# Optimization experiments

Measured on AMD Instinct MI355X. Metric: run time of the kernel, lower is better.

Reference implementation:

```python
import jax, jax.numpy as jnp
import numpy as np

DIM = 1024
N_HEADS = 16
HEAD_DIM = DIM // N_HEADS
SPARSITY = 0.8
SCALE = HEAD_DIM ** -0.5


def setup_inputs() -> dict:
    key = jax.random.key(0)
    ks = jax.random.split(key, 9)
    B, S = 2, 2048
    std = DIM ** -0.5
    return {
        "x": jax.random.normal(ks[0], (B, S, DIM), dtype=jnp.float32),
        "wq": jax.random.normal(ks[1], (DIM, DIM), dtype=jnp.float32) * std,
        "bq": jnp.zeros((DIM,), dtype=jnp.float32),
        "wk": jax.random.normal(ks[2], (DIM, DIM), dtype=jnp.float32) * std,
        "bk": jnp.zeros((DIM,), dtype=jnp.float32),
        "wv": jax.random.normal(ks[3], (DIM, DIM), dtype=jnp.float32) * std,
        "bv": jnp.zeros((DIM,), dtype=jnp.float32),
        "wo": jax.random.normal(ks[4], (DIM, DIM), dtype=jnp.float32) * std,
        "bo": jnp.zeros((DIM,), dtype=jnp.float32),
    }


def _attn(x, wq, bq, wk, bk, wv, bv, wo, bo):
    B, S, _ = x.shape
    # torch Linear: y = x @ W.T + b
    def proj(w, b):
        y = jnp.einsum('bsd,ed->bse', x, w) + b
        return y.reshape(B, S, N_HEADS, HEAD_DIM).transpose(0, 2, 1, 3)  # [B,H,S,hd]
    q, k, v = proj(wq, bq), proj(wk, bk), proj(wv, bv)
    scores = jnp.einsum('bhqd,bhkd->bhqk', q, k) * SCALE  # [B,H,S,S]
    # top-k sparsity: keep k = max(1, int(S*(1-sparsity))) largest per row
    kk = max(1, int(S * (1.0 - SPARSITY)))
    topk_vals, topk_idx = jax.lax.top_k(scores, kk)
    sparse = jnp.full_like(scores, -jnp.inf)
    sparse = jnp.put_along_axis(sparse, topk_idx, topk_vals, axis=-1, inplace=False)
    attn = jax.nn.softmax(sparse, axis=-1)  # dropout disabled (eval)
    out = jnp.einsum('bhqk,bhkd->bhqd', attn, v)
    out = out.transpose(0, 2, 1, 3).reshape(B, S, DIM)
    out = jnp.einsum('bsd,ed->bse', out, wo) + bo
    return out, attn


def reference(x, wq, bq, wk, bk, wv, bv, wo, bo):
    return _attn(x, wq, bq, wk, bk, wv, bv, wo, bo)
```

## Files before the change

### kernel.cpp

```cpp
#include <hip/hip_runtime.h>
#include <hip/hip_bf16.h>

#define DIMN 1024
#define NH 16
#define HD 64
#define SEQ 2048
#define BATCH 2
#define BHN (BATCH*NH)
#define MROWS (BATCH*SEQ)
#define KKEEP 409
#define SCALEF 0.125f
#define QROWS 16

typedef __attribute__((ext_vector_type(8))) short short8;
typedef __attribute__((ext_vector_type(4))) short short4v;
typedef __attribute__((ext_vector_type(4))) float f32x4;

#define MFMA(a,b,c) __builtin_amdgcn_mfma_f32_16x16x32_bf16(a,b,c,0,0,0)


static __device__ __forceinline__ short f2bf(float f) {
    __hip_bfloat16 h = __float2bfloat16(f);
    return *reinterpret_cast<short*>(&h);
}
static __device__ __forceinline__ float bf2f(short s) {
    __hip_bfloat16 h = *reinterpret_cast<__hip_bfloat16*>(&s);
    return __bfloat162float(h);
}
static __device__ __forceinline__ short8 ld8(const short* p) {
    return *reinterpret_cast<const short8*>(p);
}
static __device__ __forceinline__ float keyf(unsigned u) {
    unsigned fu = (u & 0x80000000u) ? (u ^ 0x80000000u) : ~u;
    return __uint_as_float(fu);
}
static __device__ __forceinline__ size_t tidx(int row, int k) {
    return (size_t)(row >> 4) * 16384 + (size_t)(k >> 5) * 512
         + ((((k >> 3) & 3) * 16 + (row & 15)) * 8) + (k & 7);
}

__global__ void conv_hilo_t(const float* __restrict__ in,
                            short* __restrict__ hi, short* __restrict__ lo, int rows) {
    const int total = rows * 256;
    for (int idx = blockIdx.x * blockDim.x + threadIdx.x; idx < total;
         idx += gridDim.x * blockDim.x) {
        const int row = idx >> 8;
        const int k = (idx & 255) * 4;
        float4 v = *reinterpret_cast<const float4*>(in + (size_t)row * DIMN + k);
        short4v h, l;
        #pragma unroll
        for (int j = 0; j < 4; ++j) {
            float f = (&v.x)[j];
            short hb = f2bf(f);
            h[j] = hb;
            l[j] = f2bf(f - bf2f(hb));
        }
        const size_t o = tidx(row, k);
        *reinterpret_cast<short4v*>(hi + o) = h;
        *reinterpret_cast<short4v*>(lo + o) = l;
    }
}

__global__ void conv_bf16_t(const float* __restrict__ in,
                            short* __restrict__ out, int rows) {
    const int total = rows * 256;
    for (int idx = blockIdx.x * blockDim.x + threadIdx.x; idx < total;
         idx += gridDim.x * blockDim.x) {
        const int row = idx >> 8;
        const int k = (idx & 255) * 4;
        float4 v = *reinterpret_cast<const float4*>(in + (size_t)row * DIMN + k);
        short4v o;
        o[0] = f2bf(v.x); o[1] = f2bf(v.y); o[2] = f2bf(v.z); o[3] = f2bf(v.w);
        *reinterpret_cast<short4v*>(out + tidx(row, k)) = o;
    }
}

__global__ __launch_bounds__(256) void qk_mfma(
    const short* __restrict__ xh, const short* __restrict__ xl,
    const short* __restrict__ wqh, const short* __restrict__ wql, const float* __restrict__ bq,
    const short* __restrict__ wkh, const short* __restrict__ wkl, const float* __restrict__ bk,
    short* __restrict__ qhi, short* __restrict__ qlo,
    short* __restrict__ khi, short* __restrict__ klo)
{
    const int z = blockIdx.z;
    const short* wh = z ? wkh : wqh;
    const short* wl = z ? wkl : wql;
    const float* bias = z ? bk : bq;
    short* dhi = z ? khi : qhi;
    short* dlo = z ? klo : qlo;

    const int tid  = threadIdx.x;
    const int wv_  = tid >> 6, lane = tid & 63;
    const int r    = lane & 15, kg = lane >> 4;
    const int m_base = blockIdx.x * 128 + wv_ * 32;
    const int n_base = blockIdx.y * 64;
    const int mtile0 = blockIdx.x * 8 + wv_ * 2;
    const int ntile0 = blockIdx.y * 4;

    f32x4 acc[2][4] = {};

    for (int ks = 0; ks < 32; ++ks) {
        short8 ah0 = ld8(xh + (size_t)mtile0 * 16384 + ks * 512 + lane * 8);
        short8 al0 = ld8(xl + (size_t)mtile0 * 16384 + ks * 512 + lane * 8);
        short8 ah1 = ld8(xh + (size_t)(mtile0 + 1) * 16384 + ks * 512 + lane * 8);
        short8 al1 = ld8(xl + (size_t)(mtile0 + 1) * 16384 + ks * 512 + lane * 8);
        #pragma unroll
        for (int nf = 0; nf < 4; ++nf) {
            short8 bh = ld8(wh + (size_t)(ntile0 + nf) * 16384 + ks * 512 + lane * 8);
            short8 bl = ld8(wl + (size_t)(ntile0 + nf) * 16384 + ks * 512 + lane * 8);
            acc[0][nf] = MFMA(ah0, bh, acc[0][nf]);
            acc[0][nf] = MFMA(ah0, bl, acc[0][nf]);
            acc[0][nf] = MFMA(al0, bh, acc[0][nf]);
            acc[1][nf] = MFMA(ah1, bh, acc[1][nf]);
            acc[1][nf] = MFMA(ah1, bl, acc[1][nf]);
            acc[1][nf] = MFMA(al1, bh, acc[1][nf]);
        }
    }

    const int h = blockIdx.y;
    #pragma unroll
    for (int mf = 0; mf < 2; ++mf)
        #pragma unroll
        for (int nf = 0; nf < 4; ++nf)
            #pragma unroll
            for (int i = 0; i < 4; ++i) {
                const int m  = m_base + mf * 16 + kg * 4 + i;
                const int nn = n_base + nf * 16 + r;
                const float val = acc[mf][nf][i] + bias[nn];
                const int b_ = m >> 11, s = m & 2047;
                const int hd = nf * 16 + r;
                const size_t idx = (size_t)(b_ * NH + h) * 131072
                    + (size_t)(s >> 4) * 1024 + (hd >> 5) * 512
                    + ((((hd >> 3) & 3) * 16 + (s & 15)) * 8) + (hd & 7);
                const short hb = f2bf(val);
                dhi[idx] = hb;
                dlo[idx] = f2bf(val - bf2f(hb));
            }
}

__global__ __launch_bounds__(256) void v_mfma(
    const short* __restrict__ xh, const short* __restrict__ xl,
    const short* __restrict__ wvb, const float* __restrict__ bv,
    short* __restrict__ vt)
{
    const int tid  = threadIdx.x;
    const int wv_  = tid >> 6, lane = tid & 63;
    const int r    = lane & 15, kg = lane >> 4;
    const int m_base = blockIdx.x * 128 + wv_ * 32;
    const int n_base = blockIdx.y * 64;
    const int mtile0 = blockIdx.x * 8 + wv_ * 2;
    const int ntile0 = blockIdx.y * 4;

    f32x4 acc[2][4] = {};

    for (int ks = 0; ks < 32; ++ks) {
        short8 ah0 = ld8(xh + (size_t)mtile0 * 16384 + ks * 512 + lane * 8);
        short8 al0 = ld8(xl + (size_t)mtile0 * 16384 + ks * 512 + lane * 8);
        short8 ah1 = ld8(xh + (size_t)(mtile0 + 1) * 16384 + ks * 512 + lane * 8);
        short8 al1 = ld8(xl + (size_t)(mtile0 + 1) * 16384 + ks * 512 + lane * 8);
        #pragma unroll
        for (int nf = 0; nf < 4; ++nf) {
            short8 b = ld8(wvb + (size_t)(ntile0 + nf) * 16384 + ks * 512 + lane * 8);
            acc[0][nf] = MFMA(ah0, b, acc[0][nf]);
            acc[0][nf] = MFMA(al0, b, acc[0][nf]);
            acc[1][nf] = MFMA(ah1, b, acc[1][nf]);
            acc[1][nf] = MFMA(al1, b, acc[1][nf]);
        }
    }

    const int h = blockIdx.y;
    #pragma unroll
    for (int mf = 0; mf < 2; ++mf)
        #pragma unroll
        for (int nf = 0; nf < 4; ++nf)
            #pragma unroll
            for (int i = 0; i < 4; ++i) {
                const int m  = m_base + mf * 16 + kg * 4 + i;
                const int nn = n_base + nf * 16 + r;
                const float val = acc[mf][nf][i] + bv[nn];
                const int b_ = m >> 11, s = m & 2047;
                const int hd = nf * 16 + r;
                const size_t idx = (size_t)(b_ * NH + h) * 131072
                    + (size_t)(hd >> 4) * 32768 + (size_t)(s >> 5) * 512
                    + ((((s >> 3) & 3) * 16 + (hd & 15)) * 8) + (s & 7);
                vt[idx] = f2bf(val);
            }
}

__global__ __launch_bounds__(512, 4) void fused_attn(
    const short* __restrict__ qh, const short* __restrict__ ql,
    const short* __restrict__ kh, const short* __restrict__ kl,
    const short* __restrict__ vtb, float* __restrict__ attn,
    short* __restrict__ ctxt)
{
    __shared__ __align__(16) char smem[32768];
    float* CT = (float*)(smem + 16384);

    const int tid = threadIdx.x;
    const int w   = tid >> 6, lane = tid & 63;
    const int r   = lane & 15, kg = lane >> 4;

    const int bid  = blockIdx.x;
    const int xcd  = bid & 7;
    const int slot = bid >> 3;
    const int bh   = xcd + 8 * (slot >> 7);
    const int qt   = slot & 127;
    const int q0   = qt * QROWS;

    const size_t qtbase = (size_t)bh * 131072 + (size_t)qt * 1024 + lane * 8;
    short8 a0h = ld8(qh + qtbase),       a0l = ld8(ql + qtbase);
    short8 a1h = ld8(qh + qtbase + 512), a1l = ld8(ql + qtbase + 512);

    unsigned u[2][32];

    auto STAGE = [&](int c, float* buf) {
        #pragma unroll
        for (int tt = 0; tt < 2; ++tt) {
            const int stile = c * 16 + w + 8 * tt;
            const size_t tb = (size_t)bh * 131072 + (size_t)stile * 1024 + lane * 8;
            short8 b0h = ld8(kh + tb);
            short8 b0l = ld8(kl + tb);
            short8 b1h = ld8(kh + tb + 512);
            short8 b1l = ld8(kl + tb + 512);
            f32x4 accA = {0.f, 0.f, 0.f, 0.f};
            f32x4 accB = {0.f, 0.f, 0.f, 0.f};
            accA = MFMA(a0h, b0h, accA);
            accB = MFMA(a1h, b1h, accB);
            accA = MFMA(a0h, b0l, accA);
            accB = MFMA(a1h, b1l, accB);
            accA = MFMA(a0l, b0h, accA);
            accB = MFMA(a1l, b1h, accB);
            const int j0c = (w + 8 * tt) * 16;
            #pragma unroll
            for (int i = 0; i < 4; ++i)
                buf[(kg * 4 + i) * 256 + j0c + r] = (accA[i] + accB[i]) * SCALEF;
        }
    };

    STAGE(0, (float*)smem);
    __syncthreads();
    #pragma unroll
    for (int c = 0; c < 8; ++c) {
        float* cur = (float*)(smem + ((c & 1) ? 16384 : 0));
        float* nxt = (float*)(smem + ((c & 1) ? 0 : 16384));
        if (c + 1 < 8) STAGE(c + 1, nxt);
        #pragma unroll
        for (int rr = 0; rr < 2; ++rr) {
            const float* src = cur + (w + 8 * rr) * 256;
            f32x4 v4 = *reinterpret_cast<const f32x4*>(src + lane * 4);
            #pragma unroll
            for (int q_ = 0; q_ < 4; ++q_) {
                unsigned fu = __float_as_uint(v4[q_]);
                u[rr][c * 4 + q_] = (fu & 0x80000000u) ? ~fu : (fu | 0x80000000u);
            }
        }
        __syncthreads();
    }

    float inv[2];
    #pragma unroll
    for (int rr = 0; rr < 2; ++rr) {
        unsigned cur = 0;
        for (int bit = 31; bit >= 0; --bit) {
            const unsigned cand = cur | (1u << bit);
            int cnt = 0;
            #pragma unroll
            for (int jj = 0; jj < 32; ++jj)
                cnt += __popcll(__ballot(u[rr][jj] >= cand));
            if (cnt >= KKEEP) {
                cur = cand;
                if (cnt == KKEEP) break;
            }
        }
        unsigned mu = 0;
        #pragma unroll
        for (int jj = 0; jj < 32; ++jj) mu = (u[rr][jj] > mu) ? u[rr][jj] : mu;
        #pragma unroll
        for (int off = 32; off; off >>= 1) {
            unsigned o = (unsigned)__shfl_xor((int)mu, off);
            mu = (o > mu) ? o : mu;
        }
        const float m = keyf(mu);
        float denom = 0.f;
        #pragma unroll
        for (int jj = 0; jj < 32; ++jj) {
            const unsigned ue = u[rr][jj];
            const float e = (ue >= cur) ? __expf(keyf(ue) - m) : 0.f;
            u[rr][jj] = __float_as_uint(e);
            denom += e;
        }
        #pragma unroll
        for (int off = 32; off; off >>= 1) denom += __shfl_xor(denom, off);
        inv[rr] = 1.0f / denom;
    }

    const int khf = w >> 2;
    const int swzw = (w & 7) << 4;
    const int swzr = (r & 7) << 4;
    f32x4 acc = {0.f, 0.f, 0.f, 0.f};

    auto EWRITE = [&](int c, char* Ebase) {
        #pragma unroll
        for (int rr = 0; rr < 2; ++rr) {
            const int row = w + 8 * rr;
            const float iv = inv[rr];
            short4v pb;
            pb[0] = f2bf(__uint_as_float(u[rr][c * 4 + 0]) * iv);
            pb[1] = f2bf(__uint_as_float(u[rr][c * 4 + 1]) * iv);
            pb[2] = f2bf(__uint_as_float(u[rr][c * 4 + 2]) * iv);
            pb[3] = f2bf(__uint_as_float(u[rr][c * 4 + 3]) * iv);
            *reinterpret_cast<short4v*>(
                Ebase + row * 512 + ((lane * 8) ^ swzw)) = pb;
        }
    };
    auto PVSTEP = [&](int c, const char* Ebase) {
        const size_t vbase = (size_t)bh * 131072 + (size_t)(w & 3) * 32768
                           + (size_t)(c * 8 + khf * 4) * 512 + lane * 8;
        const char* Eb2 = Ebase + r * 512;
        #pragma unroll
        for (int ks = 0; ks < 4; ++ks) {
            const int kk = khf * 4 + ks;
            short8 pa = *reinterpret_cast<const short8*>(
                Eb2 + ((kk * 64 + kg * 16) ^ swzr));
            short8 vb = ld8(vtb + vbase + ks * 512);
            acc = MFMA(pa, vb, acc);
        }
    };

    EWRITE(0, smem);
    __syncthreads();
    #pragma unroll
    for (int c = 0; c < 8; ++c) {
        char* curE = smem + ((c & 1) ? 8192 : 0);
        char* nxtE = smem + ((c & 1) ? 0 : 8192);
        if (c + 1 < 8) EWRITE(c + 1, nxtE);
        PVSTEP(c, curE);
        __syncthreads();
    }

    const int dt = w & 3;
    if (khf == 1) {
        #pragma unroll
        for (int i = 0; i < 4; ++i) CT[(kg * 4 + i) * 64 + dt * 16 + r] = acc[i];
    }
    __syncthreads();
    if (khf == 0) {
        const int b_ = bh >> 4, h = bh & 15;
        const size_t base = (size_t)(b_ * 128 + qt) * 16384
                          + (size_t)(h * 2 + (dt >> 1)) * 512;
        #pragma unroll
        for (int i = 0; i < 4; ++i) {
            const int lrow = kg * 4 + i;
            const float val = acc[i] + CT[lrow * 64 + dt * 16 + r];
            ctxt[base + ((((dt * 2 + (r >> 3)) & 3) * 16 + lrow) * 8) + (r & 7)]
                = f2bf(val);
        }
    }

    #pragma unroll
    for (int rr = 0; rr < 2; ++rr) {
        const int row = w + 8 * rr;
        const float iv = inv[rr];
        float* arow = attn + ((size_t)bh * SEQ + q0 + row) * SEQ + lane * 4;
        #pragma unroll
        for (int c = 0; c < 8; ++c) {
            f32x4 pv;
            pv[0] = __uint_as_float(u[rr][c * 4 + 0]) * iv;
            pv[1] = __uint_as_float(u[rr][c * 4 + 1]) * iv;
            pv[2] = __uint_as_float(u[rr][c * 4 + 2]) * iv;
            pv[3] = __uint_as_float(u[rr][c * 4 + 3]) * iv;
            __builtin_nontemporal_store(
                pv, reinterpret_cast<f32x4*>(arow + c * 256));
        }
    }
}

__global__ __launch_bounds__(256) void out_mfma(
    const short* __restrict__ ctxt, const short* __restrict__ wob,
    const float* __restrict__ bo, float* __restrict__ out)
{
    const int tid = threadIdx.x;
    const int w_  = tid >> 6, lane = tid & 63;
    const int r   = lane & 15, kg = lane >> 4;
    const int m_base = blockIdx.x * 128 + w_ * 32;
    const int n_base = blockIdx.y * 64;
    const int mtile0 = blockIdx.x * 8 + w_ * 2;
    const int ntile0 = blockIdx.y * 4;

    f32x4 acc[2][4] = {};

    for (int ks = 0; ks < 32; ++ks) {
        short8 a0 = ld8(ctxt + (size_t)mtile0 * 16384 + ks * 512 + lane * 8);
        short8 a1 = ld8(ctxt + (size_t)(mtile0 + 1) * 16384 + ks * 512 + lane * 8);
        #pragma unroll
        for (int nf = 0; nf < 4; ++nf) {
            short8 b = ld8(wob + (size_t)(ntile0 + nf) * 16384 + ks * 512 + lane * 8);
            acc[0][nf] = MFMA(a0, b, acc[0][nf]);
            acc[1][nf] = MFMA(a1, b, acc[1][nf]);
        }
    }

    #pragma unroll
    for (int mf = 0; mf < 2; ++mf)
        #pragma unroll
        for (int nf = 0; nf < 4; ++nf)
            #pragma unroll
            for (int i = 0; i < 4; ++i) {
                const int m  = m_base + mf * 16 + kg * 4 + i;
                const int nn = n_base + nf * 16 + r;
                out[(size_t)m * DIMN + nn] = acc[mf][nf][i] + bo[nn];
            }
}

extern "C" void kernel_launch(void* const* d_in, const int* in_sizes, int n_in,
                              void* d_out, int out_size, void* d_ws, size_t ws_size,
                              hipStream_t stream) {
    const float* x  = (const float*)d_in[0];
    const float* wq = (const float*)d_in[1];
    const float* bq = (const float*)d_in[2];
    const float* wk = (const float*)d_in[3];
    const float* bk = (const float*)d_in[4];
    const float* wv = (const float*)d_in[5];
    const float* bv = (const float*)d_in[6];
    const float* wo = (const float*)d_in[7];
    const float* bo = (const float*)d_in[8];

    float* out  = (float*)d_out;
    float* attn = out + (size_t)MROWS * DIMN;

    short* xhi = (short*)attn;
    short* xlo = xhi + (size_t)MROWS * DIMN;
    short* wqh = xlo + (size_t)MROWS * DIMN;
    short* wql = wqh + (size_t)DIMN * DIMN;
    short* wkh = wql + (size_t)DIMN * DIMN;
    short* wkl = wkh + (size_t)DIMN * DIMN;
    short* wvb = wkl + (size_t)DIMN * DIMN;

    const size_t QKV = (size_t)BHN * SEQ * HD;
    short* qhi = (short*)d_ws;
    short* qlo = qhi + QKV;
    short* khi = qlo + QKV;
    short* klo = khi + QKV;
    short* vt  = klo + QKV;
    short* ctx = vt  + QKV;
    short* wob = ctx + QKV;

    conv_hilo_t<<<2048, 256, 0, stream>>>(x,  xhi, xlo, MROWS);
    conv_hilo_t<<<1024, 256, 0, stream>>>(wq, wqh, wql, DIMN);
    conv_hilo_t<<<1024, 256, 0, stream>>>(wk, wkh, wkl, DIMN);
    conv_bf16_t<<<1024, 256, 0, stream>>>(wv, wvb, DIMN);
    conv_bf16_t<<<1024, 256, 0, stream>>>(wo, wob, DIMN);

    qk_mfma<<<dim3(MROWS / 128, DIMN / 64, 2), 256, 0, stream>>>(
        xhi, xlo, wqh, wql, bq, wkh, wkl, bk, qhi, qlo, khi, klo);
    v_mfma<<<dim3(MROWS / 128, DIMN / 64), 256, 0, stream>>>(
        xhi, xlo, wvb, bv, vt);

    fused_attn<<<dim3(SEQ / QROWS * BHN), 512, 0, stream>>>(
        qhi, qlo, khi, klo, vt, attn, ctx);

    out_mfma<<<dim3(MROWS / 128, DIMN / 64), 256, 0, stream>>>(ctx, wob, bo, out);
}
```

Measured before the change: 428.0 us.

## Merge conversion and QKV launches; double fused-attention chunk size

The five fp32-to-bf16 conversion launches become one grid-strided kernel that dispatches on blockIdx.y, and the QK and V projection kernels merge into one launch with a third z-slice for V. This cuts launch overhead and lets the V projection overlap with Q/K. In fused_attn the score staging and PV chunks double from 256 to 512 keys, halving the loop trip counts and barriers. The cost is doubling shared memory to 64KB, which may lower the occupancy targeted by launch_bounds(512,4).

```diff
diff --git a/kernel.cpp b/kernel.cpp
--- a/kernel.cpp
+++ b/kernel.cpp
@@ -39,8 +39,8 @@
          + ((((k >> 3) & 3) * 16 + (row & 15)) * 8) + (k & 7);
 }
 
-__global__ void conv_hilo_t(const float* __restrict__ in,
-                            short* __restrict__ hi, short* __restrict__ lo, int rows) {
+static __device__ __forceinline__ void conv_hilo_body(
+    const float* in, short* hi, short* lo, int rows) {
     const int total = rows * 256;
     for (int idx = blockIdx.x * blockDim.x + threadIdx.x; idx < total;
          idx += gridDim.x * blockDim.x) {
@@ -60,9 +60,8 @@
         *reinterpret_cast<short4v*>(lo + o) = l;
     }
 }
-
-__global__ void conv_bf16_t(const float* __restrict__ in,
-                            short* __restrict__ out, int rows) {
+static __device__ __forceinline__ void conv_bf16_body(
+    const float* in, short* out, int rows) {
     const int total = rows * 256;
     for (int idx = blockIdx.x * blockDim.x + threadIdx.x; idx < total;
          idx += gridDim.x * blockDim.x) {
@@ -74,21 +73,34 @@
         *reinterpret_cast<short4v*>(out + tidx(row, k)) = o;
     }
 }
-
-__global__ __launch_bounds__(256) void qk_mfma(
+__global__ void conv_all(
+    const float* __restrict__ x, const float* __restrict__ wq,
+    const float* __restrict__ wk, const float* __restrict__ wv,
+    const float* __restrict__ wo,
+    short* __restrict__ xhi, short* __restrict__ xlo,
+    short* __restrict__ wqh, short* __restrict__ wql,
+    short* __restrict__ wkh, short* __restrict__ wkl,
+    short* __restrict__ wvb, short* __restrict__ wob)
+{
+    switch (blockIdx.y) {
+        case 0: conv_hilo_body(x,  xhi, xlo, MROWS); break;
+        case 1: conv_hilo_body(wq, wqh, wql, DIMN);  break;
+        case 2: conv_hilo_body(wk, wkh, wkl, DIMN);  break;
+        case 3: conv_bf16_body(wv, wvb, DIMN);       break;
+        default: conv_bf16_body(wo, wob, DIMN);      break;
+    }
+}
+
+__global__ __launch_bounds__(256) void qkv_mfma(
     const short* __restrict__ xh, const short* __restrict__ xl,
     const short* __restrict__ wqh, const short* __restrict__ wql, const float* __restrict__ bq,
     const short* __restrict__ wkh, const short* __restrict__ wkl, const float* __restrict__ bk,
+    const short* __restrict__ wvb, const float* __restrict__ bv,
     short* __restrict__ qhi, short* __restrict__ qlo,
-    short* __restrict__ khi, short* __restrict__ klo)
+    short* __restrict__ khi, short* __restrict__ klo,
+    short* __restrict__ vt)
 {
     const int z = blockIdx.z;
-    const short* wh = z ? wkh : wqh;
-    const short* wl = z ? wkl : wql;
-    const float* bias = z ? bk : bq;
-    short* dhi = z ? khi : qhi;
-    short* dlo = z ? klo : qlo;
-
     const int tid  = threadIdx.x;
     const int wv_  = tid >> 6, lane = tid & 63;
     const int r    = lane & 15, kg = lane >> 4;
@@ -96,95 +108,86 @@
     const int n_base = blockIdx.y * 64;
     const int mtile0 = blockIdx.x * 8 + wv_ * 2;
     const int ntile0 = blockIdx.y * 4;
+    const int h = blockIdx.y;
 
     f32x4 acc[2][4] = {};
 
-    for (int ks = 0; ks < 32; ++ks) {
-        short8 ah0 = ld8(xh + (size_t)mtile0 * 16384 + ks * 512 + lane * 8);
-        short8 al0 = ld8(xl + (size_t)mtile0 * 16384 + ks * 512 + lane * 8);
-        short8 ah1 = ld8(xh + (size_t)(mtile0 + 1) * 16384 + ks * 512 + lane * 8);
-        short8 al1 = ld8(xl + (size_t)(mtile0 + 1) * 16384 + ks * 512 + lane * 8);
-        #pragma unroll
-        for (int nf = 0; nf < 4; ++nf) {
-            short8 bh = ld8(wh + (size_t)(ntile0 + nf) * 16384 + ks * 512 + lane * 8);
-            short8 bl = ld8(wl + (size_t)(ntile0 + nf) * 16384 + ks * 512 + lane * 8);
-            acc[0][nf] = MFMA(ah0, bh, acc[0][nf]);
-            acc[0][nf] = MFMA(ah0, bl, acc[0][nf]);
-            acc[0][nf] = MFMA(al0, bh, acc[0][nf]);
-            acc[1][nf] = MFMA(ah1, bh, acc[1][nf]);
-            acc[1][nf] = MFMA(ah1, bl, acc[1][nf]);
-            acc[1][nf] = MFMA(al1, bh, acc[1][nf]);
-        }
-    }
-
-    const int h = blockIdx.y;
-    #pragma unroll
-    for (int mf = 0; mf < 2; ++mf)
-        #pragma unroll
-        for (int nf = 0; nf < 4; ++nf)
-            #pragma unroll
-            for (int i = 0; i < 4; ++i) {
-                const int m  = m_base + mf * 16 + kg * 4 + i;
-                const int nn = n_base + nf * 16 + r;
-                const float val = acc[mf][nf][i] + bias[nn];
-                const int b_ = m >> 11, s = m & 2047;
-                const int hd = nf * 16 + r;
-                const size_t idx = (size_t)(b_ * NH + h) * 131072
-                    + (size_t)(s >> 4) * 1024 + (hd >> 5) * 512
-                    + ((((hd >> 3) & 3) * 16 + (s & 15)) * 8) + (hd & 7);
-                const short hb = f2bf(val);
-                dhi[idx] = hb;
-                dlo[idx] = f2bf(val - bf2f(hb));
-            }
-}
-
-__global__ __launch_bounds__(256) void v_mfma(
-    const short* __restrict__ xh, const short* __restrict__ xl,
-    const short* __restrict__ wvb, const float* __restrict__ bv,
-    short* __restrict__ vt)
-{
-    const int tid  = threadIdx.x;
-    const int wv_  = tid >> 6, lane = tid & 63;
-    const int r    = lane & 15, kg = lane >> 4;
-    const int m_base = blockIdx.x * 128 + wv_ * 32;
-    const int n_base = blockIdx.y * 64;
-    const int mtile0 = blockIdx.x * 8 + wv_ * 2;
-    const int ntile0 = blockIdx.y * 4;
-
-    f32x4 acc[2][4] = {};
-
-    for (int ks = 0; ks < 32; ++ks) {
-        short8 ah0 = ld8(xh + (size_t)mtile0 * 16384 + ks * 512 + lane * 8);
-        short8 al0 = ld8(xl + (size_t)mtile0 * 16384 + ks * 512 + lane * 8);
-        short8 ah1 = ld8(xh + (size_t)(mtile0 + 1) * 16384 + ks * 512 + lane * 8);
-        short8 al1 = ld8(xl + (size_t)(mtile0 + 1) * 16384 + ks * 512 + lane * 8);
-        #pragma unroll
-        for (int nf = 0; nf < 4; ++nf) {
-            short8 b = ld8(wvb + (size_t)(ntile0 + nf) * 16384 + ks * 512 + lane * 8);
-            acc[0][nf] = MFMA(ah0, b, acc[0][nf]);
-            acc[0][nf] = MFMA(al0, b, acc[0][nf]);
-            acc[1][nf] = MFMA(ah1, b, acc[1][nf]);
-            acc[1][nf] = MFMA(al1, b, acc[1][nf]);
-        }
-    }
-
-    const int h = blockIdx.y;
-    #pragma unroll
-    for (int mf = 0; mf < 2; ++mf)
-        #pragma unroll
-        for (int nf = 0; nf < 4; ++nf)
-            #pragma unroll
-            for (int i = 0; i < 4; ++i) {
-                const int m  = m_base + mf * 16 + kg * 4 + i;
-                const int nn = n_base + nf * 16 + r;
-                const float val = acc[mf][nf][i] + bv[nn];
-                const int b_ = m >> 11, s = m & 2047;
-                const int hd = nf * 16 + r;
-                const size_t idx = (size_t)(b_ * NH + h) * 131072
-                    + (size_t)(hd >> 4) * 32768 + (size_t)(s >> 5) * 512
-                    + ((((s >> 3) & 3) * 16 + (hd & 15)) * 8) + (s & 7);
-                vt[idx] = f2bf(val);
-            }
+    if (z < 2) {
+        const short* wh = z ? wkh : wqh;
+        const short* wl = z ? wkl : wql;
+        const float* bias = z ? bk : bq;
+        short* dhi = z ? khi : qhi;
+        short* dlo = z ? klo : qlo;
+
+        for (int ks = 0; ks < 32; ++ks) {
+            short8 ah0 = ld8(xh + (size_t)mtile0 * 16384 + ks * 512 + lane * 8);
+            short8 al0 = ld8(xl + (size_t)mtile0 * 16384 + ks * 512 + lane * 8);
+            short8 ah1 = ld8(xh + (size_t)(mtile0 + 1) * 16384 + ks * 512 + lane * 8);
+            short8 al1 = ld8(xl + (size_t)(mtile0 + 1) * 16384 + ks * 512 + lane * 8);
+            #pragma unroll
+            for (int nf = 0; nf < 4; ++nf) {
+                short8 bh = ld8(wh + (size_t)(ntile0 + nf) * 16384 + ks * 512 + lane * 8);
+                short8 bl = ld8(wl + (size_t)(ntile0 + nf) * 16384 + ks * 512 + lane * 8);
+                acc[0][nf] = MFMA(ah0, bh, acc[0][nf]);
+                acc[0][nf] = MFMA(ah0, bl, acc[0][nf]);
+                acc[0][nf] = MFMA(al0, bh, acc[0][nf]);
+                acc[1][nf] = MFMA(ah1, bh, acc[1][nf]);
+                acc[1][nf] = MFMA(ah1, bl, acc[1][nf]);
+                acc[1][nf] = MFMA(al1, bh, acc[1][nf]);
+            }
+        }
+
+        #pragma unroll
+        for (int mf = 0; mf < 2; ++mf)
+            #pragma unroll
+            for (int nf = 0; nf < 4; ++nf)
+                #pragma unroll
+                for (int i = 0; i < 4; ++i) {
+                    const int m  = m_base + mf * 16 + kg * 4 + i;
+                    const int nn = n_base + nf * 16 + r;
+                    const float val = acc[mf][nf][i] + bias[nn];
+                    const int b_ = m >> 11, s = m & 2047;
+                    const int hd = nf * 16 + r;
+                    const size_t idx = (size_t)(b_ * NH + h) * 131072
+                        + (size_t)(s >> 4) * 1024 + (hd >> 5) * 512
+                        + ((((hd >> 3) & 3) * 16 + (s & 15)) * 8) + (hd & 7);
+                    const short hb = f2bf(val);
+                    dhi[idx] = hb;
+                    dlo[idx] = f2bf(val - bf2f(hb));
+                }
+    } else {
+        for (int ks = 0; ks < 32; ++ks) {
+            short8 ah0 = ld8(xh + (size_t)mtile0 * 16384 + ks * 512 + lane * 8);
+            short8 al0 = ld8(xl + (size_t)mtile0 * 16384 + ks * 512 + lane * 8);
+            short8 ah1 = ld8(xh + (size_t)(mtile0 + 1) * 16384 + ks * 512 + lane * 8);
+            short8 al1 = ld8(xl + (size_t)(mtile0 + 1) * 16384 + ks * 512 + lane * 8);
+            #pragma unroll
+            for (int nf = 0; nf < 4; ++nf) {
+                short8 b = ld8(wvb + (size_t)(ntile0 + nf) * 16384 + ks * 512 + lane * 8);
+                acc[0][nf] = MFMA(ah0, b, acc[0][nf]);
+                acc[0][nf] = MFMA(al0, b, acc[0][nf]);
+                acc[1][nf] = MFMA(ah1, b, acc[1][nf]);
+                acc[1][nf] = MFMA(al1, b, acc[1][nf]);
+            }
+        }
+
+        #pragma unroll
+        for (int mf = 0; mf < 2; ++mf)
+            #pragma unroll
+            for (int nf = 0; nf < 4; ++nf)
+                #pragma unroll
+                for (int i = 0; i < 4; ++i) {
+                    const int m  = m_base + mf * 16 + kg * 4 + i;
+                    const int nn = n_base + nf * 16 + r;
+                    const float val = acc[mf][nf][i] + bv[nn];
+                    const int b_ = m >> 11, s = m & 2047;
+                    const int hd = nf * 16 + r;
+                    const size_t idx = (size_t)(b_ * NH + h) * 131072
+                        + (size_t)(hd >> 4) * 32768 + (size_t)(s >> 5) * 512
+                        + ((((s >> 3) & 3) * 16 + (hd & 15)) * 8) + (s & 7);
+                    vt[idx] = f2bf(val);
+                }
+    }
 }
 
 __global__ __launch_bounds__(512, 4) void fused_attn(
@@ -193,8 +196,8 @@
     const short* __restrict__ vtb, float* __restrict__ attn,
     short* __restrict__ ctxt)
 {
-    __shared__ __align__(16) char smem[32768];
-    float* CT = (float*)(smem + 16384);
+    __shared__ __align__(16) char smem[65536];
+    float* CT = (float*)(smem + 32768);
 
     const int tid = threadIdx.x;
     const int w   = tid >> 6, lane = tid & 63;
@@ -215,8 +218,8 @@
 
     auto STAGE = [&](int c, float* buf) {
         #pragma unroll
-        for (int tt = 0; tt < 2; ++tt) {
-            const int stile = c * 16 + w + 8 * tt;
+        for (int tt = 0; tt < 4; ++tt) {
+            const int stile = c * 32 + w + 8 * tt;
             const size_t tb = (size_t)bh * 131072 + (size_t)stile * 1024 + lane * 8;
             short8 b0h = ld8(kh + tb);
             short8 b0l = ld8(kl + tb);
@@ -233,25 +236,29 @@
             const int j0c = (w + 8 * tt) * 16;
             #pragma unroll
             for (int i = 0; i < 4; ++i)
-                buf[(kg * 4 + i) * 256 + j0c + r] = (accA[i] + accB[i]) * SCALEF;
+                buf[(kg * 4 + i) * 512 + j0c + r] = (accA[i] + accB[i]) * SCALEF;
         }
     };
 
     STAGE(0, (float*)smem);
     __syncthreads();
     #pragma unroll
-    for (int c = 0; c < 8; ++c) {
-        float* cur = (float*)(smem + ((c & 1) ? 16384 : 0));
-        float* nxt = (float*)(smem + ((c & 1) ? 0 : 16384));
-        if (c + 1 < 8) STAGE(c + 1, nxt);
+    for (int c = 0; c < 4; ++c) {
+        float* cur = (float*)(smem + ((c & 1) ? 32768 : 0));
+        float* nxt = (float*)(smem + ((c & 1) ? 0 : 32768));
+        if (c + 1 < 4) STAGE(c + 1, nxt);
         #pragma unroll
         for (int rr = 0; rr < 2; ++rr) {
-            const float* src = cur + (w + 8 * rr) * 256;
-            f32x4 v4 = *reinterpret_cast<const f32x4*>(src + lane * 4);
-            #pragma unroll
-            for (int q_ = 0; q_ < 4; ++q_) {
-                unsigned fu = __float_as_uint(v4[q_]);
-                u[rr][c * 4 + q_] = (fu & 0x80000000u) ? ~fu : (fu | 0x80000000u);
+            const float* src = cur + (w + 8 * rr) * 512;
+            #pragma unroll
+            for (int g = 0; g < 2; ++g) {
+                f32x4 v4 = *reinterpret_cast<const f32x4*>(src + g * 256 + lane * 4);
+                #pragma unroll
+                for (int q_ = 0; q_ < 4; ++q_) {
+                    unsigned fu = __float_as_uint(v4[q_]);
+                    u[rr][c * 8 + g * 4 + q_] =
+                        (fu & 0x80000000u) ? ~fu : (fu | 0x80000000u);
+                }
             }
         }
         __syncthreads();
@@ -304,22 +311,25 @@
         for (int rr = 0; rr < 2; ++rr) {
             const int row = w + 8 * rr;
             const float iv = inv[rr];
-            short4v pb;
-            pb[0] = f2bf(__uint_as_float(u[rr][c * 4 + 0]) * iv);
-            pb[1] = f2bf(__uint_as_float(u[rr][c * 4 + 1]) * iv);
-            pb[2] = f2bf(__uint_as_float(u[rr][c * 4 + 2]) * iv);
-            pb[3] = f2bf(__uint_as_float(u[rr][c * 4 + 3]) * iv);
-            *reinterpret_cast<short4v*>(
-                Ebase + row * 512 + ((lane * 8) ^ swzw)) = pb;
+            #pragma unroll
+            for (int g = 0; g < 2; ++g) {
+                short4v pb;
+                pb[0] = f2bf(__uint_as_float(u[rr][c * 8 + g * 4 + 0]) * iv);
+                pb[1] = f2bf(__uint_as_float(u[rr][c * 8 + g * 4 + 1]) * iv);
+                pb[2] = f2bf(__uint_as_float(u[rr][c * 8 + g * 4 + 2]) * iv);
+                pb[3] = f2bf(__uint_as_float(u[rr][c * 8 + g * 4 + 3]) * iv);
+                *reinterpret_cast<short4v*>(
+                    Ebase + row * 1024 + ((g * 512 + lane * 8) ^ swzw)) = pb;
+            }
         }
     };
     auto PVSTEP = [&](int c, const char* Ebase) {
         const size_t vbase = (size_t)bh * 131072 + (size_t)(w & 3) * 32768
-                           + (size_t)(c * 8 + khf * 4) * 512 + lane * 8;
-        const char* Eb2 = Ebase + r * 512;
-        #pragma unroll
-        for (int ks = 0; ks < 4; ++ks) {
-            const int kk = khf * 4 + ks;
+                           + (size_t)(c * 16 + khf * 8) * 512 + lane * 8;
+        const char* Eb2 = Ebase + r * 1024;
+        #pragma unroll
+        for (int ks = 0; ks < 8; ++ks) {
+            const int kk = khf * 8 + ks;
             short8 pa = *reinterpret_cast<const short8*>(
                 Eb2 + ((kk * 64 + kg * 16) ^ swzr));
             short8 vb = ld8(vtb + vbase + ks * 512);
@@ -330,10 +340,10 @@
     EWRITE(0, smem);
     __syncthreads();
     #pragma unroll
-    for (int c = 0; c < 8; ++c) {
-        char* curE = smem + ((c & 1) ? 8192 : 0);
-        char* nxtE = smem + ((c & 1) ? 0 : 8192);
-        if (c + 1 < 8) EWRITE(c + 1, nxtE);
+    for (int c = 0; c < 4; ++c) {
+        char* curE = smem + ((c & 1) ? 16384 : 0);
+        char* nxtE = smem + ((c & 1) ? 0 : 16384);
+        if (c + 1 < 4) EWRITE(c + 1, nxtE);
         PVSTEP(c, curE);
         __syncthreads();
     }
@@ -363,15 +373,17 @@
         const float iv = inv[rr];
         float* arow = attn + ((size_t)bh * SEQ + q0 + row) * SEQ + lane * 4;
         #pragma unroll
-        for (int c = 0; c < 8; ++c) {
-            f32x4 pv;
-            pv[0] = __uint_as_float(u[rr][c * 4 + 0]) * iv;
-            pv[1] = __uint_as_float(u[rr][c * 4 + 1]) * iv;
-            pv[2] = __uint_as_float(u[rr][c * 4 + 2]) * iv;
-            pv[3] = __uint_as_float(u[rr][c * 4 + 3]) * iv;
-            __builtin_nontemporal_store(
-                pv, reinterpret_cast<f32x4*>(arow + c * 256));
-        }
+        for (int c = 0; c < 4; ++c)
+            #pragma unroll
+            for (int g = 0; g < 2; ++g) {
+                f32x4 pv;
+                pv[0] = __uint_as_float(u[rr][c * 8 + g * 4 + 0]) * iv;
+                pv[1] = __uint_as_float(u[rr][c * 8 + g * 4 + 1]) * iv;
+                pv[2] = __uint_as_float(u[rr][c * 8 + g * 4 + 2]) * iv;
+                pv[3] = __uint_as_float(u[rr][c * 8 + g * 4 + 3]) * iv;
+                __builtin_nontemporal_store(
+                    pv, reinterpret_cast<f32x4*>(arow + c * 512 + g * 256));
+            }
     }
 }
 
@@ -445,16 +457,12 @@
     short* ctx = vt  + QKV;
     short* wob = ctx + QKV;
 
-    conv_hilo_t<<<2048, 256, 0, stream>>>(x,  xhi, xlo, MROWS);
-    conv_hilo_t<<<1024, 256, 0, stream>>>(wq, wqh, wql, DIMN);
-    conv_hilo_t<<<1024, 256, 0, stream>>>(wk, wkh, wkl, DIMN);
-    conv_bf16_t<<<1024, 256, 0, stream>>>(wv, wvb, DIMN);
-    conv_bf16_t<<<1024, 256, 0, stream>>>(wo, wob, DIMN);
-
-    qk_mfma<<<dim3(MROWS / 128, DIMN / 64, 2), 256, 0, stream>>>(
-        xhi, xlo, wqh, wql, bq, wkh, wkl, bk, qhi, qlo, khi, klo);
-    v_mfma<<<dim3(MROWS / 128, DIMN / 64), 256, 0, stream>>>(
-        xhi, xlo, wvb, bv, vt);
+    conv_all<<<dim3(512, 5), 256, 0, stream>>>(
+        x, wq, wk, wv, wo, xhi, xlo, wqh, wql, wkh, wkl, wvb, wob);
+
+    qkv_mfma<<<dim3(MROWS / 128, DIMN / 64, 3), 256, 0, stream>>>(
+        xhi, xlo, wqh, wql, bq, wkh, wkl, bk, wvb, bv,
+        qhi, qlo, khi, klo, vt);
 
     fused_attn<<<dim3(SEQ / QROWS * BHN), 512, 0, stream>>>(
         qhi, qlo, khi, klo, vt, attn, ctx);
```

Measured after the change: 408.7 us (median of 2 runs). 1.05x faster.
